# Optimization experiments

Hardware: AMD Instinct MI355X
Metric: run time of the kernel (lower is better)

The kernel has to match this reference:

```python
import jax, jax.numpy as jnp
import numpy as np

NLEFT = 8
NRIGHT = 8
D = 768
L = 512
R = 512


def _make_lengths(key, n_attr, total):
    # random positive-ish lengths summing exactly to `total`
    w = jax.random.randint(key, (n_attr,), 1, 64).astype(jnp.float32)
    c = jnp.floor(jnp.cumsum(w) / jnp.sum(w) * total).astype(jnp.int32)
    lens = jnp.diff(jnp.concatenate([jnp.zeros((1,), jnp.int32), c]))
    return lens


def setup_inputs() -> dict:
    key = jax.random.key(0)
    ks = jax.random.split(key, 16)
    std = 0.05
    inp = {
        "left_embeddings": jax.random.normal(ks[0], (L, D), jnp.float32),
        "right_embeddings": jax.random.normal(ks[1], (R, D), jnp.float32),
        "left_attrs_len": _make_lengths(ks[2], NLEFT, L),
        "right_attrs_len": _make_lengths(ks[3], NRIGHT, R),
        # HighwayNet token matching params (input_size=D)
        "hw_tok_Wn": jax.random.normal(ks[4], (D, D), jnp.float32) * std,
        "hw_tok_bn": jnp.zeros((D,), jnp.float32),
        "hw_tok_Wg": jax.random.normal(ks[5], (D, D), jnp.float32) * std,
        "hw_tok_bg": jnp.full((D,), -2.0, jnp.float32),
        "lin_tok_W": jax.random.normal(ks[6], (D, 1), jnp.float32) * std,
        "lin_tok_b": jnp.zeros((1,), jnp.float32),
        "attr_emb_left": jax.random.normal(ks[7], (NLEFT, D), jnp.float32) * std,
        "attr_emb_right": jax.random.normal(ks[8], (NRIGHT, D), jnp.float32) * std,
        # entity matching highway (input_size = (nleft+nright)*D)
        "hw_ent_Wn": jax.random.normal(ks[9], ((NLEFT + NRIGHT) * D, (NLEFT + NRIGHT) * D), jnp.float32) * 0.01,
        "hw_ent_bn": jnp.zeros(((NLEFT + NRIGHT) * D,), jnp.float32),
        "hw_ent_Wg": jax.random.normal(ks[10], ((NLEFT + NRIGHT) * D, (NLEFT + NRIGHT) * D), jnp.float32) * 0.01,
        "hw_ent_bg": jnp.full(((NLEFT + NRIGHT) * D,), -2.0, jnp.float32),
        "lin_ent_W": jax.random.normal(ks[11], ((NLEFT + NRIGHT) * D, 2), jnp.float32) * 0.01,
        "lin_ent_b": jnp.zeros((2,), jnp.float32),
        "empty_attr_res": jax.random.normal(ks[12], (D,), jnp.float32) * std,
    }
    return inp


def _highway(x, Wn, bn, Wg, bg):
    h = jax.nn.relu(x @ Wn + bn)
    g = jax.nn.sigmoid(x @ Wg + bg)
    return g * h + (1.0 - g) * x


def _token_matching(left, right, Wn, bn, Wg, bg, Wl, bl):
    # For each left token i: compare = |left_i - right| -> [R, D]
    # weights = softmax over R of linear(highway(compare)); take row at argmax.
    cmp = jnp.abs(left[:, None, :] - right[None, :, :])  # [L, R, D]
    hw = _highway(cmp, Wn, bn, Wg, bg)                    # [L, R, D]
    scores = (hw @ Wl).squeeze(-1) + bl[0]                # [L, R]
    # softmax over R is monotone; argmax of softmax == argmax of scores
    idx = jnp.argmax(scores, axis=1)                      # [L]
    return jnp.take_along_axis(cmp, idx[:, None, None], axis=1).squeeze(1)  # [L, D]


def _attribute_matching(tokens, field_emb, cmp_res, lens, empty_res, n_attr, n_tok):
    # segment ids per token from lens
    starts = jnp.cumsum(lens) - lens                      # [n_attr]
    seg = jnp.sum(jnp.arange(n_tok)[:, None] >= (starts + lens)[None, :], axis=1)  # [n_tok]
    seg = jnp.clip(seg, 0, n_attr - 1)
    # scores = tokens @ field_emb[seg]
    logits = jnp.einsum('td,td->t', tokens, field_emb[seg])  # [n_tok]
    # ragged softmax per segment
    seg_max = jax.ops.segment_max(logits, seg, num_segments=n_attr)
    ex = jnp.exp(logits - seg_max[seg])
    denom = jax.ops.segment_sum(ex, seg, num_segments=n_attr)
    w = ex / denom[seg]                                    # [n_tok]
    res = jax.ops.segment_sum(w[:, None] * cmp_res, seg, num_segments=n_attr)  # [n_attr, D]
    empty = (lens == 0)
    return jnp.where(empty[:, None], empty_res[None, :], res)


def reference(left_embeddings, right_embeddings, left_attrs_len, right_attrs_len,
              hw_tok_Wn, hw_tok_bn, hw_tok_Wg, hw_tok_bg, lin_tok_W, lin_tok_b,
              attr_emb_left, attr_emb_right,
              hw_ent_Wn, hw_ent_bn, hw_ent_Wg, hw_ent_bg, lin_ent_W, lin_ent_b,
              empty_attr_res):
    lcmp = _token_matching(left_embeddings, right_embeddings,
                           hw_tok_Wn, hw_tok_bn, hw_tok_Wg, hw_tok_bg, lin_tok_W, lin_tok_b)
    rcmp = _token_matching(right_embeddings, left_embeddings,
                           hw_tok_Wn, hw_tok_bn, hw_tok_Wg, hw_tok_bg, lin_tok_W, lin_tok_b)
    lrep = _attribute_matching(left_embeddings, attr_emb_left, lcmp,
                               left_attrs_len, empty_attr_res, NLEFT, L)
    rrep = _attribute_matching(right_embeddings, attr_emb_right, rcmp,
                               right_attrs_len, empty_attr_res, NRIGHT, R)
    concat = jnp.concatenate([lrep, rrep], axis=0).reshape(1, -1)  # [1, (nl+nr)*D]
    hw = _highway(concat, hw_ent_Wn, hw_ent_bn, hw_ent_Wg, hw_ent_bg)
    logits = hw @ lin_ent_W + lin_ent_b
    return jax.nn.softmax(logits, axis=1).flatten()
```

## Files before the change

kernel.cpp:

```cpp
#include <hip/hip_runtime.h>
#include <cmath>

#define NL 8
#define NR 8
#define DIM 768
#define LTOK 512
#define RTOK 512
#define EDIM 12288
#define KST 32

typedef unsigned short u16;
typedef __bf16 bf16x8 __attribute__((ext_vector_type(8)));
typedef float  f32x16 __attribute__((ext_vector_type(16)));

#define WARR 589824

__device__ __forceinline__ void splitbf(float c, u16& hi, u16& lo) {
    __bf16 h = (__bf16)c;
    __bf16 l = (__bf16)(c - (float)h);
    hi = __builtin_bit_cast(u16, h);
    lo = __builtin_bit_cast(u16, l);
}

__device__ __forceinline__ void gll16(const void* gsrc, void* lds) {
    __builtin_amdgcn_global_load_lds(
        (const __attribute__((address_space(1))) unsigned int*)gsrc,
        (__attribute__((address_space(3))) unsigned int*)lds, 16, 0, 0);
}

__global__ __launch_bounds__(256) void wsplit_kernel(
    const float* __restrict__ Wn, const float* __restrict__ Wg, u16* __restrict__ out)
{
    const int gid = blockIdx.x * 256 + threadIdx.x;
    const int d  = gid % DIM;
    const int kg = gid / DIM;
    u16 hn[8], ln[8], hg[8], lg2[8];
#pragma unroll
    for (int e = 0; e < 8; ++e) {
        splitbf(Wn[(size_t)(kg * 8 + e) * DIM + d], hn[e], ln[e]);
        splitbf(Wg[(size_t)(kg * 8 + e) * DIM + d], hg[e], lg2[e]);
    }
    const size_t fo = ((size_t)kg * DIM + d) * 8;
    *(uint4*)&out[fo]            = *(uint4*)hn;
    *(uint4*)&out[WARR + fo]     = *(uint4*)ln;
    *(uint4*)&out[2 * WARR + fo] = *(uint4*)hg;
    *(uint4*)&out[3 * WARR + fo] = *(uint4*)lg2;
}

__global__ __launch_bounds__(256) void ltrans_kernel(
    const float* __restrict__ Lg, float* __restrict__ Lt)
{
    __shared__ float tile[32][33];
    const int tx  = threadIdx.x & 31;
    const int ty4 = threadIdx.x >> 5;
    const int k0 = blockIdx.x * 32, i0 = blockIdx.y * 32;
#pragma unroll
    for (int rr = 0; rr < 4; ++rr) {
        int iy = ty4 * 4 + rr;
        tile[iy][tx] = Lg[(size_t)(i0 + iy) * DIM + k0 + tx];
    }
    __syncthreads();
#pragma unroll
    for (int rr = 0; rr < 4; ++rr) {
        int ky = ty4 * 4 + rr;
        Lt[(size_t)(k0 + ky) * LTOK + i0 + tx] = tile[tx][ky];
    }
}

__global__ __launch_bounds__(512, 2) void scores_kernel(
    const float* __restrict__ Lg, const float* __restrict__ Rg,
    const float* __restrict__ Lt,
    const u16* __restrict__ wfrag,
    const float* __restrict__ bn, const float* __restrict__ bg,
    const float* __restrict__ Wl,
    float* __restrict__ scores)
{
    __shared__ u16   wLDS[3 * 8192];
    __shared__ float lLDS[2 * 2048];
    __shared__ float rLDS[8 * 768];

    const int t    = threadIdx.x;
    const int lane = t & 63;
    const int wid  = t >> 6;
    const int l31  = lane & 31;
    const int kh   = lane >> 5;
    const int i0   = blockIdx.x * 64;
    const int j0   = blockIdx.y * 8;
    const int j    = j0 + wid;

    const ptrdiff_t WSTEP = (ptrdiff_t)4 * DIM * 8;
    const ptrdiff_t WROLL = (ptrdiff_t)(64 - 92 * DIM) * 8;

    const u16* wp[2];
#pragma unroll
    for (int it = 0; it < 2; ++it) {
        const int c = it * 8 + wid;
        wp[it] = wfrag + (size_t)(c >> 2) * WARR + ((size_t)(c & 3) * DIM + lane) * 8;
    }

    const float* apL = Lt + (size_t)(t >> 4) * LTOK + i0 + (t & 15) * 4;

    gll16(apL, lLDS + wid * 256);
#pragma unroll
    for (int it = 0; it < 2; ++it)
        gll16(wp[it], wLDS + (it * 8 + wid) * 512);
#pragma unroll
    for (int r = 0; r < 3; ++r)
        gll16(Rg + (size_t)j0 * DIM + (size_t)(r * 512 + t) * 4,
              rLDS + r * 2048 + wid * 256);
#pragma unroll
    for (int it = 0; it < 2; ++it)
        gll16(wp[it] + WSTEP, wLDS + 8192 + (it * 8 + wid) * 512);

#pragma unroll
    for (int it = 0; it < 2; ++it) wp[it] += 2 * WSTEP;
    apL += 16384;

    asm volatile("s_waitcnt vmcnt(2)" ::: "memory");
    __builtin_amdgcn_s_barrier();

    float sacc[2][16];
#pragma unroll
    for (int tile = 0; tile < 2; ++tile)
#pragma unroll
        for (int r = 0; r < 16; ++r) sacc[tile][r] = 0.f;

    f32x16 acc[2][2][2];
#pragma unroll
    for (int tile = 0; tile < 2; ++tile)
#pragma unroll
        for (int mat = 0; mat < 2; ++mat)
#pragma unroll
            for (int nd = 0; nd < 2; ++nd)
#pragma unroll
                for (int r = 0; r < 16; ++r) acc[tile][mat][nd][r] = 0.f;

    int ksC = 0, k0C = 0, dg = 0, lRd = 0;
    const u16* wRd = wLDS;
    u16*       wWr = wLDS + 2 * 8192;
    const u16* const wEndc = wLDS + 3 * 8192;

#pragma unroll 1
    for (int s = 0; s < 288; ++s) {
        auto phase = [&](int kk) {
            const float* rrow = rLDS + wid * 768 + k0C + kh * 8;
            float rv[8];
#pragma unroll
            for (int e = 0; e < 8; e += 2) {
                float2 p = *(const float2*)(rrow + kk * 16 + e);
                rv[e] = p.x; rv[e + 1] = p.y;
            }
            bf16x8 ah[2], al[2];
            const float* lb = lLDS + lRd * 2048 + kh * 512;
#pragma unroll
            for (int tile = 0; tile < 2; ++tile) {
                const float* lp = lb + kk * 1024 + tile * 32 + l31;
#pragma unroll
                for (int e = 0; e < 8; ++e) {
                    float c = fabsf(lp[e * 64] - rv[e]);
                    __bf16 h = (__bf16)c;
                    ah[tile][e] = h;
                    al[tile][e] = (__bf16)(c - (float)h);
                }
            }
            __builtin_amdgcn_s_setprio(1);
#pragma unroll
            for (int mat = 0; mat < 2; ++mat)
#pragma unroll
                for (int nd = 0; nd < 2; ++nd) {
                    const int base = (mat * 2) * 2048 + (kk * 2 + kh) * 512
                                   + (nd * 32 + l31) * 8;
                    bf16x8 whi = *(const bf16x8*)&wRd[base];
                    bf16x8 wlo = *(const bf16x8*)&wRd[base + 2048];
#pragma unroll
                    for (int tile = 0; tile < 2; ++tile) {
                        acc[tile][mat][nd] = __builtin_amdgcn_mfma_f32_32x32x16_bf16(
                            ah[tile], whi, acc[tile][mat][nd], 0, 0, 0);
                        acc[tile][mat][nd] = __builtin_amdgcn_mfma_f32_32x32x16_bf16(
                            al[tile], whi, acc[tile][mat][nd], 0, 0, 0);
                        acc[tile][mat][nd] = __builtin_amdgcn_mfma_f32_32x32x16_bf16(
                            ah[tile], wlo, acc[tile][mat][nd], 0, 0, 0);
                    }
                }
            __builtin_amdgcn_s_setprio(0);
        };

        if (s < 287) {
            gll16(apL, lLDS + (lRd ^ 1) * 2048 + wid * 256);
            apL += (ksC == 22) ? (ptrdiff_t)-376832 : (ptrdiff_t)16384;
        }
        phase(0);

        if (s < 286) {
#pragma unroll
            for (int it = 0; it < 2; ++it)
                gll16(wp[it], wWr + (it * 8 + wid) * 512);
            const ptrdiff_t adv = (ksC == 21) ? WROLL : WSTEP;
#pragma unroll
            for (int it = 0; it < 2; ++it) wp[it] += adv;
        }
        phase(1);

        if (ksC == 23) {
#pragma unroll
            for (int nd = 0; nd < 2; ++nd) {
                const int dd = dg + nd * 32 + l31;
                const float bnv = bn[dd], bgv = bg[dd], wlv = Wl[dd];
                const float rvv = Rg[(size_t)j * DIM + dd];
#pragma unroll
                for (int tile = 0; tile < 2; ++tile)
#pragma unroll
                    for (int r = 0; r < 16; ++r) {
                        const int m = (r & 3) + 8 * (r >> 2) + 4 * kh;
                        const int i = i0 + tile * 32 + m;
                        float h  = fmaxf(acc[tile][0][nd][r] + bnv, 0.f);
                        float g  = 1.f / (1.f + __expf(-(acc[tile][1][nd][r] + bgv)));
                        float cc = fabsf(Lg[(size_t)i * DIM + dd] - rvv);
                        sacc[tile][r] = fmaf(wlv, fmaf(g, h - cc, cc), sacc[tile][r]);
                    }
            }
#pragma unroll
            for (int tile = 0; tile < 2; ++tile)
#pragma unroll
                for (int mat = 0; mat < 2; ++mat)
#pragma unroll
                    for (int nd = 0; nd < 2; ++nd)
#pragma unroll
                        for (int r = 0; r < 16; ++r) acc[tile][mat][nd][r] = 0.f;
        }

        if (s == 286) { asm volatile("s_waitcnt vmcnt(0)" ::: "memory"); }
        else         { asm volatile("s_waitcnt vmcnt(2)" ::: "memory"); }
        __builtin_amdgcn_s_barrier();

        lRd ^= 1;
        wRd += 8192; if (wRd == wEndc) wRd = wLDS;
        wWr += 8192; if (wWr == (u16*)wEndc) wWr = wLDS;
        ++ksC; k0C += KST;
        if (ksC == 24) { ksC = 0; k0C = 0; dg += 64; }
    }

#pragma unroll
    for (int tile = 0; tile < 2; ++tile)
#pragma unroll
        for (int r = 0; r < 16; ++r) {
            float v = sacc[tile][r];
            v += __shfl_xor(v, 1);  v += __shfl_xor(v, 2);
            v += __shfl_xor(v, 4);  v += __shfl_xor(v, 8);
            v += __shfl_xor(v, 16);
            if (l31 == 0) {
                const int m = (r & 3) + 8 * (r >> 2) + 4 * kh;
                scores[(size_t)(i0 + tile * 32 + m) * RTOK + j] = v;
            }
        }
}

__global__ __launch_bounds__(64) void argmax_kernel(
    const float* __restrict__ scores, int* __restrict__ idxL, int* __restrict__ idxR)
{
    const int b = blockIdx.x;
    const int t = threadIdx.x;
    const bool isRow = (b < LTOK);
    const int  n = b & (LTOK - 1);

    float best = -INFINITY;
    int   bidx = 0x7fffffff;
    for (int s = t; s < 512; s += 64) {
        float v = isRow ? scores[n * RTOK + s] : scores[s * RTOK + n];
        if (v > best) { best = v; bidx = s; }
    }
#pragma unroll
    for (int off = 32; off; off >>= 1) {
        float ob = __shfl_down(best, off);
        int   oi = __shfl_down(bidx, off);
        if (ob > best || (ob == best && oi < bidx)) { best = ob; bidx = oi; }
    }
    if (t == 0) (isRow ? idxL : idxR)[n] = bidx;
}

__global__ __launch_bounds__(256) void build_cmp_kernel(
    const float* __restrict__ Lg, const float* __restrict__ Rg,
    const int* __restrict__ idxL, const int* __restrict__ idxR,
    float* __restrict__ lcmp, float* __restrict__ rcmp)
{
    const int b = blockIdx.x;
    const int t = threadIdx.x;
    if (b < LTOK) {
        const float* a = Lg + b * DIM;
        const float* c = Rg + idxL[b] * DIM;
        for (int d = t; d < DIM; d += 256) lcmp[b * DIM + d] = fabsf(a[d] - c[d]);
    } else {
        const int jj = b - LTOK;
        const float* a = Rg + jj * DIM;
        const float* c = Lg + idxR[jj] * DIM;
        for (int d = t; d < DIM; d += 256) rcmp[jj * DIM + d] = fabsf(a[d] - c[d]);
    }
}

__global__ __launch_bounds__(256) void attr_match_kernel(
    const float* __restrict__ Lg, const float* __restrict__ Rg,
    const float* __restrict__ lcmp, const float* __restrict__ rcmp,
    const int* __restrict__ lensL, const int* __restrict__ lensR,
    const float* __restrict__ embL, const float* __restrict__ embR,
    const float* __restrict__ emptyRes,
    float* __restrict__ x)
{
    __shared__ float logits[512];
    __shared__ float red[256];

    const int b    = blockIdx.x;
    const int side = b >> 3;
    const int a    = b & 7;
    const int t    = threadIdx.x;

    const int*   lens = side ? lensR : lensL;
    const float* toks = side ? Rg   : Lg;
    const float* cmp  = side ? rcmp : lcmp;
    const float* femb = (side ? embR : embL) + a * DIM;
    float* outp = x + (side * 8 + a) * DIM;

    int start = 0;
    for (int q = 0; q < a; ++q) start += lens[q];
    const int len = lens[a];

    if (len == 0) {
        for (int d = t; d < DIM; d += 256) outp[d] = emptyRes[d];
        return;
    }

    for (int tok = t; tok < len; tok += 256) {
        const float* tr = toks + (start + tok) * DIM;
        float s = 0.f;
        for (int d = 0; d < DIM; ++d) s = fmaf(tr[d], femb[d], s);
        logits[tok] = s;
    }
    __syncthreads();

    float m = -INFINITY;
    for (int tok = t; tok < len; tok += 256) m = fmaxf(m, logits[tok]);
    red[t] = m; __syncthreads();
    for (int off = 128; off; off >>= 1) {
        if (t < off) red[t] = fmaxf(red[t], red[t + off]);
        __syncthreads();
    }
    m = red[0]; __syncthreads();

    float sum = 0.f;
    for (int tok = t; tok < len; tok += 256) {
        float e = expf(logits[tok] - m);
        logits[tok] = e;
        sum += e;
    }
    red[t] = sum; __syncthreads();
    for (int off = 128; off; off >>= 1) {
        if (t < off) red[t] += red[t + off];
        __syncthreads();
    }
    const float inv = 1.f / red[0];
    __syncthreads();

    for (int d = t; d < DIM; d += 256) {
        float accv = 0.f;
        for (int tok = 0; tok < len; ++tok)
            accv = fmaf(logits[tok] * inv, cmp[(start + tok) * DIM + d], accv);
        outp[d] = accv;
    }
}

__global__ __launch_bounds__(256) void ent_partial_kernel(
    const float* __restrict__ Wn, const float* __restrict__ Wg,
    const float* __restrict__ x, float* __restrict__ partial)
{
    __shared__ float xs[384];
    const int ob   = blockIdx.x;
    const int slab = blockIdx.y;
    const int mat  = blockIdx.z;
    const float* W = mat ? Wg : Wn;
    const int t  = threadIdx.x;
    const int o0 = ob * 1024 + t * 4;
    const int in0 = slab * 384;

    for (int i = t; i < 384; i += 256) xs[i] = x[in0 + i];
    __syncthreads();

    float4 acc = {0.f, 0.f, 0.f, 0.f};
    for (int in = 0; in < 384; ++in) {
        const float  xv = xs[in];
        const float4 w  = *(const float4*)(W + (size_t)(in0 + in) * EDIM + o0);
        acc.x = fmaf(xv, w.x, acc.x);
        acc.y = fmaf(xv, w.y, acc.y);
        acc.z = fmaf(xv, w.z, acc.z);
        acc.w = fmaf(xv, w.w, acc.w);
    }
    *(float4*)(partial + ((size_t)mat * 32 + slab) * EDIM + o0) = acc;
}

__global__ __launch_bounds__(256) void ent_reduce_kernel(
    const float* __restrict__ partial, float* __restrict__ hsum)
{
    const int mat = blockIdx.y;
    const int o   = blockIdx.x * 1024 + threadIdx.x * 4;
    float4 acc = {0.f, 0.f, 0.f, 0.f};
    for (int s = 0; s < 32; ++s) {
        const float4 p = *(const float4*)(partial + ((size_t)mat * 32 + s) * EDIM + o);
        acc.x += p.x; acc.y += p.y; acc.z += p.z; acc.w += p.w;
    }
    *(float4*)(hsum + (size_t)mat * EDIM + o) = acc;
}

__global__ __launch_bounds__(256) void finalize_kernel(
    const float* __restrict__ hsum, const float* __restrict__ x,
    const float* __restrict__ bn, const float* __restrict__ bg,
    const float* __restrict__ Wl2, const float* __restrict__ bl2,
    float* __restrict__ out)
{
    __shared__ float r0[256], r1[256];
    const int t = threadIdx.x;
    float l0 = 0.f, l1 = 0.f;
    for (int d = t; d < EDIM; d += 256) {
        float h  = fmaxf(hsum[d] + bn[d], 0.f);
        float gv = 1.f / (1.f + expf(-(hsum[EDIM + d] + bg[d])));
        float hw = gv * h + (1.f - gv) * x[d];
        l0 = fmaf(hw, Wl2[d * 2 + 0], l0);
        l1 = fmaf(hw, Wl2[d * 2 + 1], l1);
    }
    r0[t] = l0; r1[t] = l1; __syncthreads();
    for (int off = 128; off; off >>= 1) {
        if (t < off) { r0[t] += r0[t + off]; r1[t] += r1[t + off]; }
        __syncthreads();
    }
    if (t == 0) {
        float a = r0[0] + bl2[0];
        float b = r1[0] + bl2[1];
        float m  = fmaxf(a, b);
        float ea = expf(a - m), eb = expf(b - m);
        float inv = 1.f / (ea + eb);
        out[0] = ea * inv;
        out[1] = eb * inv;
    }
}

extern "C" void kernel_launch(void* const* d_in, const int* in_sizes, int n_in,
                              void* d_out, int out_size, void* d_ws, size_t ws_size,
                              hipStream_t stream)
{
    const float* Lg     = (const float*)d_in[0];
    const float* Rg     = (const float*)d_in[1];
    const int*   lensL  = (const int*)  d_in[2];
    const int*   lensR  = (const int*)  d_in[3];
    const float* tWn    = (const float*)d_in[4];
    const float* tbn    = (const float*)d_in[5];
    const float* tWg    = (const float*)d_in[6];
    const float* tbg    = (const float*)d_in[7];
    const float* tWl    = (const float*)d_in[8];
    const float* embL   = (const float*)d_in[10];
    const float* embR   = (const float*)d_in[11];
    const float* eWn    = (const float*)d_in[12];
    const float* ebn    = (const float*)d_in[13];
    const float* eWg    = (const float*)d_in[14];
    const float* ebg    = (const float*)d_in[15];
    const float* eWl    = (const float*)d_in[16];
    const float* ebl    = (const float*)d_in[17];
    const float* emptyR = (const float*)d_in[18];
    float* out = (float*)d_out;

    char* ws = (char*)d_ws;
    u16*   wsplit  = (u16*)ws;
    float* scores  = (float*)(ws + 4718592);
    int*   idxL    = (int*)(ws + 5767168);
    int*   idxR    = idxL + 512;
    float* xcat    = (float*)(ws + 5771264);
    float* hsum    = (float*)(ws + 5820416);
    float* Lt      = (float*)(ws + 5918720);
    float* lcmp    = (float*)ws;
    float* rcmp    = lcmp + (size_t)LTOK * DIM;
    float* partial = (float*)ws;

    wsplit_kernel<<<dim3(288), 256, 0, stream>>>(tWn, tWg, wsplit);

    ltrans_kernel<<<dim3(DIM / 32, LTOK / 32), 256, 0, stream>>>(Lg, Lt);

    scores_kernel<<<dim3(LTOK / 64, RTOK / 8), 512, 0, stream>>>(
        Lg, Rg, Lt, wsplit, tbn, tbg, tWl, scores);

    argmax_kernel<<<dim3(LTOK + RTOK), 64, 0, stream>>>(scores, idxL, idxR);

    build_cmp_kernel<<<dim3(LTOK + RTOK), 256, 0, stream>>>(
        Lg, Rg, idxL, idxR, lcmp, rcmp);

    attr_match_kernel<<<dim3(16), 256, 0, stream>>>(
        Lg, Rg, lcmp, rcmp, lensL, lensR, embL, embR, emptyR, xcat);

    ent_partial_kernel<<<dim3(EDIM / 1024, 32, 2), 256, 0, stream>>>(
        eWn, eWg, xcat, partial);

    ent_reduce_kernel<<<dim3(EDIM / 1024, 2), 256, 0, stream>>>(partial, hsum);

    finalize_kernel<<<dim3(1), 256, 0, stream>>>(
        hsum, xcat, ebn, ebg, eWl, ebl, out);
}
```

Baseline: 2.076 ms.

## Load L tiles row-major with XOR swizzle, drop transpose kernel

```diff
diff --git a/kernel.cpp b/kernel.cpp
--- a/kernel.cpp
+++ b/kernel.cpp
@@ -47,29 +47,8 @@
     *(uint4*)&out[3 * WARR + fo] = *(uint4*)lg2;
 }
 
-__global__ __launch_bounds__(256) void ltrans_kernel(
-    const float* __restrict__ Lg, float* __restrict__ Lt)
-{
-    __shared__ float tile[32][33];
-    const int tx  = threadIdx.x & 31;
-    const int ty4 = threadIdx.x >> 5;
-    const int k0 = blockIdx.x * 32, i0 = blockIdx.y * 32;
-#pragma unroll
-    for (int rr = 0; rr < 4; ++rr) {
-        int iy = ty4 * 4 + rr;
-        tile[iy][tx] = Lg[(size_t)(i0 + iy) * DIM + k0 + tx];
-    }
-    __syncthreads();
-#pragma unroll
-    for (int rr = 0; rr < 4; ++rr) {
-        int ky = ty4 * 4 + rr;
-        Lt[(size_t)(k0 + ky) * LTOK + i0 + tx] = tile[tx][ky];
-    }
-}
-
 __global__ __launch_bounds__(512, 2) void scores_kernel(
     const float* __restrict__ Lg, const float* __restrict__ Rg,
-    const float* __restrict__ Lt,
     const u16* __restrict__ wfrag,
     const float* __restrict__ bn, const float* __restrict__ bg,
     const float* __restrict__ Wl,
@@ -78,12 +57,14 @@
     __shared__ u16   wLDS[3 * 8192];
     __shared__ float lLDS[2 * 2048];
     __shared__ float rLDS[8 * 768];
+    __shared__ float saccLDS[512];
 
     const int t    = threadIdx.x;
     const int lane = t & 63;
     const int wid  = t >> 6;
     const int l31  = lane & 31;
     const int kh   = lane >> 5;
+    const int swz  = l31 & 7;
     const int i0   = blockIdx.x * 64;
     const int j0   = blockIdx.y * 8;
     const int j    = j0 + wid;
@@ -98,7 +79,8 @@
         wp[it] = wfrag + (size_t)(c >> 2) * WARR + ((size_t)(c & 3) * DIM + lane) * 8;
     }
 
-    const float* apL = Lt + (size_t)(t >> 4) * LTOK + i0 + (t & 15) * 4;
+    const float* apL = Lg + (size_t)(i0 + (t >> 3)) * DIM
+                     + (((t & 7) ^ ((t >> 3) & 7)) << 2);
 
     gll16(apL, lLDS + wid * 256);
 #pragma unroll
@@ -114,16 +96,10 @@
 
 #pragma unroll
     for (int it = 0; it < 2; ++it) wp[it] += 2 * WSTEP;
-    apL += 16384;
+    apL += KST;
 
     asm volatile("s_waitcnt vmcnt(2)" ::: "memory");
     __builtin_amdgcn_s_barrier();
-
-    float sacc[2][16];
-#pragma unroll
-    for (int tile = 0; tile < 2; ++tile)
-#pragma unroll
-        for (int r = 0; r < 16; ++r) sacc[tile][r] = 0.f;
 
     f32x16 acc[2][2][2];
 #pragma unroll
@@ -142,28 +118,32 @@
 
 #pragma unroll 1
     for (int s = 0; s < 288; ++s) {
-        auto phase = [&](int kk) {
-            const float* rrow = rLDS + wid * 768 + k0C + kh * 8;
-            float rv[8];
-#pragma unroll
-            for (int e = 0; e < 8; e += 2) {
-                float2 p = *(const float2*)(rrow + kk * 16 + e);
-                rv[e] = p.x; rv[e + 1] = p.y;
-            }
+        auto phase = [&](int kk, bool pre, bool post) {
+            const float* rrow = rLDS + wid * 768 + k0C + kh * 8 + kk * 16;
+            float4 p0 = *(const float4*)(rrow);
+            float4 p1 = *(const float4*)(rrow + 4);
+            float rv[8] = { p0.x, p0.y, p0.z, p0.w, p1.x, p1.y, p1.z, p1.w };
+
             bf16x8 ah[2], al[2];
-            const float* lb = lLDS + lRd * 2048 + kh * 512;
+            const int kqL = kk * 4 + kh * 2;
+            const float* lbase = lLDS + lRd * 2048;
 #pragma unroll
             for (int tile = 0; tile < 2; ++tile) {
-                const float* lp = lb + kk * 1024 + tile * 32 + l31;
+                const float* lrow = lbase + (tile * 32 + l31) * 32;
+                float4 q0 = *(const float4*)(lrow + ((kqL)     ^ swz) * 4);
+                float4 q1 = *(const float4*)(lrow + ((kqL + 1) ^ swz) * 4);
+                float cv[8] = { fabsf(q0.x - rv[0]), fabsf(q0.y - rv[1]),
+                                fabsf(q0.z - rv[2]), fabsf(q0.w - rv[3]),
+                                fabsf(q1.x - rv[4]), fabsf(q1.y - rv[5]),
+                                fabsf(q1.z - rv[6]), fabsf(q1.w - rv[7]) };
 #pragma unroll
                 for (int e = 0; e < 8; ++e) {
-                    float c = fabsf(lp[e * 64] - rv[e]);
-                    __bf16 h = (__bf16)c;
+                    __bf16 h = (__bf16)cv[e];
                     ah[tile][e] = h;
-                    al[tile][e] = (__bf16)(c - (float)h);
+                    al[tile][e] = (__bf16)(cv[e] - (float)h);
                 }
             }
-            __builtin_amdgcn_s_setprio(1);
+            if (pre) __builtin_amdgcn_s_setprio(1);
 #pragma unroll
             for (int mat = 0; mat < 2; ++mat)
 #pragma unroll
@@ -182,14 +162,14 @@
                             ah[tile], wlo, acc[tile][mat][nd], 0, 0, 0);
                     }
                 }
-            __builtin_amdgcn_s_setprio(0);
+            if (post) __builtin_amdgcn_s_setprio(0);
         };
 
         if (s < 287) {
             gll16(apL, lLDS + (lRd ^ 1) * 2048 + wid * 256);
-            apL += (ksC == 22) ? (ptrdiff_t)-376832 : (ptrdiff_t)16384;
+            apL += (ksC == 22) ? (ptrdiff_t)-736 : (ptrdiff_t)KST;
         }
-        phase(0);
+        phase(0, true, false);
 
         if (s < 286) {
 #pragma unroll
@@ -199,9 +179,14 @@
 #pragma unroll
             for (int it = 0; it < 2; ++it) wp[it] += adv;
         }
-        phase(1);
+        phase(1, false, true);
 
         if (ksC == 23) {
+            float sv[2][16];
+#pragma unroll
+            for (int tile = 0; tile < 2; ++tile)
+#pragma unroll
+                for (int r = 0; r < 16; ++r) sv[tile][r] = 0.f;
 #pragma unroll
             for (int nd = 0; nd < 2; ++nd) {
                 const int dd = dg + nd * 32 + l31;
@@ -216,9 +201,27 @@
                         float h  = fmaxf(acc[tile][0][nd][r] + bnv, 0.f);
                         float g  = 1.f / (1.f + __expf(-(acc[tile][1][nd][r] + bgv)));
                         float cc = fabsf(Lg[(size_t)i * DIM + dd] - rvv);
-                        sacc[tile][r] = fmaf(wlv, fmaf(g, h - cc, cc), sacc[tile][r]);
+                        sv[tile][r] = fmaf(wlv, fmaf(g, h - cc, cc), sv[tile][r]);
                     }
             }
+#pragma unroll
+            for (int tile = 0; tile < 2; ++tile)
+#pragma unroll
+                for (int r = 0; r < 16; ++r) {
+                    float v = sv[tile][r];
+                    v += __shfl_xor(v, 1);  v += __shfl_xor(v, 2);
+                    v += __shfl_xor(v, 4);  v += __shfl_xor(v, 8);
+                    v += __shfl_xor(v, 16);
+                    if (l31 == 0) {
+                        const int m = (r & 3) + 8 * (r >> 2) + 4 * kh;
+                        const int slot = wid * 64 + tile * 32 + m;
+                        if (dg == 0)        saccLDS[slot] = v;
+                        else if (dg == 704)
+                            scores[(size_t)(i0 + tile * 32 + m) * RTOK + j] =
+                                saccLDS[slot] + v;
+                        else                saccLDS[slot] += v;
+                    }
+                }
 #pragma unroll
             for (int tile = 0; tile < 2; ++tile)
 #pragma unroll
@@ -239,20 +242,6 @@
         ++ksC; k0C += KST;
         if (ksC == 24) { ksC = 0; k0C = 0; dg += 64; }
     }
-
-#pragma unroll
-    for (int tile = 0; tile < 2; ++tile)
-#pragma unroll
-        for (int r = 0; r < 16; ++r) {
-            float v = sacc[tile][r];
-            v += __shfl_xor(v, 1);  v += __shfl_xor(v, 2);
-            v += __shfl_xor(v, 4);  v += __shfl_xor(v, 8);
-            v += __shfl_xor(v, 16);
-            if (l31 == 0) {
-                const int m = (r & 3) + 8 * (r >> 2) + 4 * kh;
-                scores[(size_t)(i0 + tile * 32 + m) * RTOK + j] = v;
-            }
-        }
 }
 
 __global__ __launch_bounds__(64) void argmax_kernel(
@@ -471,17 +460,14 @@
     int*   idxR    = idxL + 512;
     float* xcat    = (float*)(ws + 5771264);
     float* hsum    = (float*)(ws + 5820416);
-    float* Lt      = (float*)(ws + 5918720);
     float* lcmp    = (float*)ws;
     float* rcmp    = lcmp + (size_t)LTOK * DIM;
     float* partial = (float*)ws;
 
     wsplit_kernel<<<dim3(288), 256, 0, stream>>>(tWn, tWg, wsplit);
 
-    ltrans_kernel<<<dim3(DIM / 32, LTOK / 32), 256, 0, stream>>>(Lg, Lt);
-
     scores_kernel<<<dim3(LTOK / 64, RTOK / 8), 512, 0, stream>>>(
-        Lg, Rg, Lt, wsplit, tbn, tbg, tWl, scores);
+        Lg, Rg, wsplit, tbn, tbg, tWl, scores);
 
     argmax_kernel<<<dim3(LTOK + RTOK), 64, 0, stream>>>(scores, idxL, idxR);
 
```

Measured after the change: 2.549 ms. +22.8%, slower.
